# Kernel optimization log

Hardware: AMD Instinct MI355X
Metric: run time of the kernel (lower is better)

The kernel has to match this reference:

```python
import jax, jax.numpy as jnp
import numpy as np

ALPHA = 0.2  # LeakyReLU negative slope
NHEADS = 3
N = 100000
DEG = 32
NFEAT = 256
NHID = 64
NCLASS = 40


def _gat_layer(x, dst, src, W, a_dst, a_src, concat):
    # SpGraphAttentionLayer: h = x @ W; e_ij = exp(-leakyrelu(a1.h_i + a2.h_j));
    # out_i = sum_j e_ij h_j / sum_j e_ij  (edge (i,j) has dst=i, src=j)
    n = x.shape[0]
    h = x @ W                                   # [N, F']
    logits = (h @ a_dst)[dst] + (h @ a_src)[src]  # [E]
    e = jnp.exp(-jax.nn.leaky_relu(logits, ALPHA))  # [E]
    denom = jax.ops.segment_sum(e, dst, num_segments=n)            # [N]
    num = jax.ops.segment_sum(e[:, None] * h[src], dst, num_segments=n)  # [N, F']
    out = num / (denom[:, None] + 1e-16)
    return jax.nn.elu(out) if concat else out


def setup_inputs() -> dict:
    key = jax.random.key(0)
    ks = jax.random.split(key, 8)
    x = jax.random.normal(ks[0], (N, NFEAT), dtype=jnp.float32)
    # random edges + self-loops so every node has at least one incoming edge
    rnd = jax.random.randint(ks[1], (2, N * DEG), 0, N, dtype=jnp.int64)
    loops = jnp.tile(jnp.arange(N, dtype=jnp.int64)[None, :], (2, 1))
    edge_index = jnp.concatenate([rnd, loops], axis=1)  # [2, E]
    s = 1.0 / np.sqrt(NFEAT)
    W = jax.random.uniform(ks[2], (NHEADS, NFEAT, NHID), jnp.float32, -s, s)
    a1 = jax.random.uniform(ks[3], (NHEADS, NHID), jnp.float32, -s, s)
    a2 = jax.random.uniform(ks[4], (NHEADS, NHID), jnp.float32, -s, s)
    s2 = 1.0 / np.sqrt(NHEADS * NHID)
    W_out = jax.random.uniform(ks[5], (NHEADS * NHID, NCLASS), jnp.float32, -s2, s2)
    a1_out = jax.random.uniform(ks[6], (NCLASS,), jnp.float32, -s2, s2)
    a2_out = jax.random.uniform(ks[7], (NCLASS,), jnp.float32, -s2, s2)
    return {"x": x, "edge_index": edge_index, "W": W, "a1": a1, "a2": a2,
            "W_out": W_out, "a1_out": a1_out, "a2_out": a2_out}


def reference(x, edge_index, W, a1, a2, W_out, a1_out, a2_out):
    # eval mode: dropout is identity
    dst, src = edge_index[0], edge_index[1]
    heads = [_gat_layer(x, dst, src, W[k], a1[k], a2[k], concat=True)
             for k in range(NHEADS)]
    h = jnp.concatenate(heads, axis=1)  # [N, NHEADS*NHID]
    out = _gat_layer(h, dst, src, W_out, a1_out, a2_out, concat=False)
    return jax.nn.elu(out)  # [N, NCLASS]
```

## Files before the change

kernel.cpp:

```cpp
#include <hip/hip_runtime.h>

#define ALPHA 0.2f
#define NFEAT 256
#define NHID 64
#define NHEADS 3
#define NCLASS 40

#define CSRB 256
#define LDSW 12512
#define NP8  (LDSW * 8)

typedef short short8 __attribute__((ext_vector_type(8)));
typedef float float4v __attribute__((ext_vector_type(4)));
typedef _Float16 half4_t __attribute__((ext_vector_type(4)));

__device__ __forceinline__ float lrelu_negexp(float x) {
    float l = fmaxf(x, 0.f) + ALPHA * fminf(x, 0.f);
    return __expf(-l);
}
__device__ __forceinline__ float elu1(float x) {
    return x > 0.f ? x : (__expf(x) - 1.f);
}
__device__ __forceinline__ unsigned short f2bf(float f) {
    unsigned int u = __float_as_uint(f);
    unsigned int r = (u + 0x7FFFu + ((u >> 16) & 1u)) >> 16;
    return (unsigned short)r;
}
__device__ __forceinline__ float bf2f(unsigned short h) {
    return __uint_as_float(((unsigned int)h) << 16);
}
__device__ __forceinline__ float rdlane_f(float v, int l) {
    return __uint_as_float((unsigned)__builtin_amdgcn_readlane((int)__float_as_uint(v), l));
}

__global__ __launch_bounds__(256) void cvt_w_k(const float* __restrict__ W,
        unsigned short* __restrict__ wthi, unsigned short* __restrict__ wtlo) {
    int i = blockIdx.x * 256 + threadIdx.x;
    if (i >= NHEADS * NHID * NFEAT) return;
    int k = i & 255, nc = (i >> 8) & 63, head = i >> 14;
    float v = W[(size_t)head * NFEAT * NHID + (size_t)k * NHID + nc];
    unsigned short hi = f2bf(v);
    unsigned short lo = f2bf(v - bf2f(hi));
    wthi[i] = hi;
    wtlo[i] = lo;
}

__global__ __launch_bounds__(256) void gemm1_mfma_k(
        const float* __restrict__ x,
        const unsigned short* __restrict__ wthi, const unsigned short* __restrict__ wtlo,
        _Float16* __restrict__ h1h, int N) {
    __shared__ unsigned short Ah[128 * 40];
    __shared__ unsigned short Al[128 * 40];
    __shared__ unsigned short Bh[192 * 40];
    __shared__ unsigned short Bl[192 * 40];
    const int tid = threadIdx.x;
    const int wave = tid >> 6, lane = tid & 63;
    const int quad = lane >> 4, l16 = lane & 15;
    const int row0 = blockIdx.x * 128;
    const int wm = (wave >> 1) * 64;
    const int wn = (wave & 1) * 96;

    float4v acc[4][6];
#pragma unroll
    for (int s = 0; s < 4; ++s)
#pragma unroll
        for (int t = 0; t < 6; ++t)
            acc[s][t] = (float4v){0.f, 0.f, 0.f, 0.f};

    for (int kc = 0; kc < NFEAT; kc += 32) {
#pragma unroll
        for (int rr = 0; rr < 2; ++rr) {
            int idx = rr * 256 + tid;
            int r = idx >> 2, kq = (idx & 3) * 8;
            int gr = row0 + r; if (gr >= N) gr = N - 1;
            const float* xp = x + (size_t)gr * NFEAT + kc + kq;
            float4 f0 = *(const float4*)xp;
            float4 f1 = *(const float4*)(xp + 4);
            ushort4 h0, h1v, l0, l1;
            h0.x = f2bf(f0.x); l0.x = f2bf(f0.x - bf2f(h0.x));
            h0.y = f2bf(f0.y); l0.y = f2bf(f0.y - bf2f(h0.y));
            h0.z = f2bf(f0.z); l0.z = f2bf(f0.z - bf2f(h0.z));
            h0.w = f2bf(f0.w); l0.w = f2bf(f0.w - bf2f(h0.w));
            h1v.x = f2bf(f1.x); l1.x = f2bf(f1.x - bf2f(h1v.x));
            h1v.y = f2bf(f1.y); l1.y = f2bf(f1.y - bf2f(h1v.y));
            h1v.z = f2bf(f1.z); l1.z = f2bf(f1.z - bf2f(h1v.z));
            h1v.w = f2bf(f1.w); l1.w = f2bf(f1.w - bf2f(h1v.w));
            *(ushort4*)&Ah[r * 40 + kq]     = h0;
            *(ushort4*)&Ah[r * 40 + kq + 4] = h1v;
            *(ushort4*)&Al[r * 40 + kq]     = l0;
            *(ushort4*)&Al[r * 40 + kq + 4] = l1;
        }
#pragma unroll
        for (int rr = 0; rr < 3; ++rr) {
            int idx = rr * 256 + tid;
            int r = idx >> 2, kq = (idx & 3) * 8;
            size_t g = (size_t)r * NFEAT + kc + kq;
            *(int4*)&Bh[r * 40 + kq] = *(const int4*)(wthi + g);
            *(int4*)&Bl[r * 40 + kq] = *(const int4*)(wtlo + g);
        }
        __syncthreads();

        short8 ah[4], al[4];
#pragma unroll
        for (int s = 0; s < 4; ++s) {
            int m = wm + s * 16 + l16;
            ah[s] = *(const short8*)&Ah[m * 40 + quad * 8];
            al[s] = *(const short8*)&Al[m * 40 + quad * 8];
        }
#pragma unroll
        for (int t = 0; t < 6; ++t) {
            int n = wn + t * 16 + l16;
            short8 bh = *(const short8*)&Bh[n * 40 + quad * 8];
            short8 bl = *(const short8*)&Bl[n * 40 + quad * 8];
#pragma unroll
            for (int s = 0; s < 4; ++s) {
                acc[s][t] = __builtin_amdgcn_mfma_f32_16x16x32_bf16(ah[s], bh, acc[s][t], 0, 0, 0);
                acc[s][t] = __builtin_amdgcn_mfma_f32_16x16x32_bf16(ah[s], bl, acc[s][t], 0, 0, 0);
                acc[s][t] = __builtin_amdgcn_mfma_f32_16x16x32_bf16(al[s], bh, acc[s][t], 0, 0, 0);
            }
        }
        __syncthreads();
    }
#pragma unroll
    for (int s = 0; s < 4; ++s) {
#pragma unroll
        for (int r = 0; r < 4; ++r) {
            int grow = row0 + wm + s * 16 + quad * 4 + r;
            if (grow < N) {
#pragma unroll
                for (int t = 0; t < 6; ++t)
                    h1h[(size_t)grow * 192 + wn + t * 16 + l16] = (_Float16)acc[s][t][r];
            }
        }
    }
}

__global__ __launch_bounds__(256) void dots1_k(const _Float16* __restrict__ h1h,
        const float* __restrict__ a1, const float* __restrict__ a2,
        float* __restrict__ ad4, float* __restrict__ as4, int N) {
    int gt = blockIdx.x * 256 + threadIdx.x;
    int wid = gt >> 6, lane = gt & 63;
    if (wid >= N) return;
    const _Float16* hr = h1h + (size_t)wid * 192;
#pragma unroll
    for (int k = 0; k < 3; ++k) {
        float v = (float)hr[k*64 + lane];
        float da = v * a1[k*64 + lane];
        float db = v * a2[k*64 + lane];
#pragma unroll
        for (int o = 32; o > 0; o >>= 1) {
            da += __shfl_down(da, o, 64);
            db += __shfl_down(db, o, 64);
        }
        if (lane == 0) { ad4[wid*4+k] = da; as4[wid*4+k] = db; }
    }
}

__global__ __launch_bounds__(256) void hist_nib_k(const int* __restrict__ dst,
        unsigned* __restrict__ partial, int E) {
    __shared__ unsigned nib[LDSW];
    const int b = blockIdx.x, tid = threadIdx.x;
    for (int i = tid; i < LDSW; i += 256) nib[i] = 0u;
    __syncthreads();
    int chunk = (E + CSRB - 1) / CSRB;
    int e0 = b * chunk, e1 = min(E, e0 + chunk);
    for (int e = e0 + tid; e < e1; e += 256) {
        int d = dst[e];
        atomicAdd(&nib[d >> 3], 1u << ((d & 7) * 4));
    }
    __syncthreads();
    unsigned* p = partial + (size_t)b * LDSW;
    for (int i = tid; i < LDSW; i += 256) p[i] = nib[i];
}

__global__ __launch_bounds__(256) void bscan_k(const unsigned* __restrict__ partial,
        unsigned char* __restrict__ prefix8, int* __restrict__ cnt, int N) {
    int w = blockIdx.x * 256 + threadIdx.x;
    if (w >= LDSW) return;
    unsigned run[8];
#pragma unroll
    for (int n = 0; n < 8; ++n) run[n] = 0u;
    for (int b = 0; b < CSRB; ++b) {
        unsigned v = partial[(size_t)b * LDSW + w];
        unsigned lo = run[0] | (run[1] << 8) | (run[2] << 16) | (run[3] << 24);
        unsigned hi = run[4] | (run[5] << 8) | (run[6] << 16) | (run[7] << 24);
        *(uint2*)(prefix8 + (size_t)b * NP8 + (size_t)w * 8) = make_uint2(lo, hi);
#pragma unroll
        for (int n = 0; n < 8; ++n) run[n] += (v >> (n * 4)) & 15u;
    }
#pragma unroll
    for (int n = 0; n < 8; ++n) {
        int idx = w * 8 + n;
        if (idx < N) cnt[idx] = (int)run[n];
    }
}

__global__ __launch_bounds__(256) void scan1_k(const int* __restrict__ cnt,
        int* __restrict__ part, int* __restrict__ sums, int N) {
    __shared__ int s[256];
    int tid = threadIdx.x, b = blockIdx.x;
    int base = b * 2048 + tid * 8;
    int v[8]; int t = 0;
#pragma unroll
    for (int i = 0; i < 8; ++i) { int idx = base + i; v[i] = (idx < N) ? cnt[idx] : 0; t += v[i]; }
    s[tid] = t; __syncthreads();
    for (int o = 1; o < 256; o <<= 1) {
        int u = (tid >= o) ? s[tid - o] : 0;
        __syncthreads();
        s[tid] += u;
        __syncthreads();
    }
    int run = s[tid] - t;
#pragma unroll
    for (int i = 0; i < 8; ++i) { int idx = base + i; if (idx < N) part[idx] = run; run += v[i]; }
    if (tid == 255) sums[b] = s[255];
}

__global__ void scan2_k(int* sums, int nb) {
    if (threadIdx.x == 0 && blockIdx.x == 0) {
        int run = 0;
        for (int i = 0; i < nb; ++i) { int t = sums[i]; sums[i] = run; run += t; }
    }
}

__global__ __launch_bounds__(256) void scan3_k(const int* __restrict__ part,
        const int* __restrict__ sums, int* __restrict__ ptr, int N, int E) {
    int i = blockIdx.x * 256 + threadIdx.x;
    if (i < N) ptr[i] = part[i] + sums[i >> 11];
    if (i == 0) ptr[N] = E;
}

__global__ __launch_bounds__(256) void scatter_nib_k(const int* __restrict__ dst,
        const int* __restrict__ src, const int* __restrict__ ptr,
        const unsigned char* __restrict__ prefix8, int* __restrict__ csr, int E) {
    __shared__ unsigned nib[LDSW];
    const int b = blockIdx.x, tid = threadIdx.x;
    for (int i = tid; i < LDSW; i += 256) nib[i] = 0u;
    __syncthreads();
    const unsigned char* pb = prefix8 + (size_t)b * NP8;
    int chunk = (E + CSRB - 1) / CSRB;
    int e0 = b * chunk, e1 = min(E, e0 + chunk);
    for (int e = e0 + tid; e < e1; e += 256) {
        int d = dst[e];
        unsigned old = atomicAdd(&nib[d >> 3], 1u << ((d & 7) * 4));
        int local = (int)((old >> ((d & 7) * 4)) & 15u);
        csr[ptr[d] + (int)pb[d] + local] = src[e];
    }
}

__global__ __launch_bounds__(256) void agg1f_k(const _Float16* __restrict__ h1h,
        const float4* __restrict__ ad4, const float4* __restrict__ as4,
        const int* __restrict__ ptr, const int* __restrict__ csr,
        _Float16* __restrict__ out1h, int N) {
    int gt = blockIdx.x * 256 + threadIdx.x;
    int wid = gt >> 6, lane = gt & 63;
    if (wid >= N) return;
    int p0 = __builtin_amdgcn_readfirstlane(ptr[wid]);
    int p1 = __builtin_amdgcn_readfirstlane(ptr[wid + 1]);
    float4 ad = ad4[wid];
    const _Float16* hb = h1h + lane;
    float acc0 = 0.f, acc1 = 0.f, acc2 = 0.f;
    float dx = 0.f, dy = 0.f, dz = 0.f;

    for (int b0 = p0; b0 < p1; b0 += 64) {
        int e = b0 + lane;
        int cnt = min(64, p1 - b0);
        int si = 0; float wx = 0.f, wy = 0.f, wz = 0.f;
        if (e < p1) {
            si = csr[e];
            float4 as = as4[si];
            wx = lrelu_negexp(ad.x + as.x);
            wy = lrelu_negexp(ad.y + as.y);
            wz = lrelu_negexp(ad.z + as.z);
            dx += wx; dy += wy; dz += wz;
        }
        int jn = cnt & ~7;
        for (int j = 0; j < jn; j += 8) {
            float va[8], vb[8], vc[8], wxr[8], wyr[8], wzr[8];
#pragma unroll
            for (int i = 0; i < 8; ++i) {
                int s = __builtin_amdgcn_readlane(si, j + i);
                wxr[i] = rdlane_f(wx, j + i);
                wyr[i] = rdlane_f(wy, j + i);
                wzr[i] = rdlane_f(wz, j + i);
                const _Float16* hp = hb + (size_t)s * 192;
                va[i] = (float)hp[0];
                vb[i] = (float)hp[64];
                vc[i] = (float)hp[128];
            }
#pragma unroll
            for (int i = 0; i < 8; ++i) {
                acc0 = fmaf(wxr[i], va[i], acc0);
                acc1 = fmaf(wyr[i], vb[i], acc1);
                acc2 = fmaf(wzr[i], vc[i], acc2);
            }
        }
        for (int j = jn; j < cnt; ++j) {
            int s = __builtin_amdgcn_readlane(si, j);
            float wxx = rdlane_f(wx, j), wyy = rdlane_f(wy, j), wzz = rdlane_f(wz, j);
            const _Float16* hp = hb + (size_t)s * 192;
            acc0 = fmaf(wxx, (float)hp[0], acc0);
            acc1 = fmaf(wyy, (float)hp[64], acc1);
            acc2 = fmaf(wzz, (float)hp[128], acc2);
        }
    }

#pragma unroll
    for (int o = 32; o > 0; o >>= 1) {
        dx += __shfl_xor(dx, o, 64);
        dy += __shfl_xor(dy, o, 64);
        dz += __shfl_xor(dz, o, 64);
    }
    size_t ob = (size_t)wid * 192;
    out1h[ob + lane]       = (_Float16)elu1(acc0 / (dx + 1e-16f));
    out1h[ob + 64 + lane]  = (_Float16)elu1(acc1 / (dy + 1e-16f));
    out1h[ob + 128 + lane] = (_Float16)elu1(acc2 / (dz + 1e-16f));
}

__global__ __launch_bounds__(256) void gemm2_k(const _Float16* __restrict__ X,
        const float* __restrict__ Wo, _Float16* __restrict__ h2h, int N) {
    __shared__ float Xs[32][193];
    __shared__ float Ws[192 * 40];
    const int tid = threadIdx.x;
    const int row0 = blockIdx.x * 32;
    for (int i = tid; i < 192 * 40; i += 256) Ws[i] = Wo[i];
    for (int i = tid; i < 32 * 48; i += 256) {
        int r = i / 48, c4 = (i % 48) * 4;
        int rr = row0 + r; if (rr >= N) rr = N - 1;
        half4_t v = *(const half4_t*)(X + (size_t)rr * 192 + c4);
        Xs[r][c4+0] = (float)v.x; Xs[r][c4+1] = (float)v.y;
        Xs[r][c4+2] = (float)v.z; Xs[r][c4+3] = (float)v.w;
    }
    __syncthreads();
    int rsub = tid >> 3;
    int f0 = (tid & 7) * 5;
    float acc[5] = {0, 0, 0, 0, 0};
    for (int c = 0; c < 192; ++c) {
        float xv = Xs[rsub][c];
#pragma unroll
        for (int j = 0; j < 5; ++j) acc[j] = fmaf(xv, Ws[c*40 + f0 + j], acc[j]);
    }
    int r = row0 + rsub;
    if (r < N) {
#pragma unroll
        for (int j = 0; j < 5; ++j) h2h[(size_t)r*64 + f0 + j] = (_Float16)acc[j];
    }
}

__global__ __launch_bounds__(256) void dots2_k(const _Float16* __restrict__ h2h,
        const float* __restrict__ a1o, const float* __restrict__ a2o,
        float* __restrict__ ad2, float* __restrict__ as2, int N) {
    int gt = blockIdx.x * 256 + threadIdx.x;
    int wid = gt >> 6, lane = gt & 63;
    if (wid >= N) return;
    float v = 0.f, w1 = 0.f, w2 = 0.f;
    if (lane < 40) { v = (float)h2h[(size_t)wid*64 + lane]; w1 = a1o[lane]; w2 = a2o[lane]; }
    float da = v * w1, db = v * w2;
#pragma unroll
    for (int o = 32; o > 0; o >>= 1) { da += __shfl_down(da, o, 64); db += __shfl_down(db, o, 64); }
    if (lane == 0) { ad2[wid] = da; as2[wid] = db; }
}

__global__ __launch_bounds__(256) void agg2f_k(const _Float16* __restrict__ h2h,
        const float* __restrict__ ad2, const float* __restrict__ as2,
        const int* __restrict__ ptr, const int* __restrict__ csr,
        float* __restrict__ out, int N) {
    int gt = blockIdx.x * 256 + threadIdx.x;
    int wid = gt >> 6, lane = gt & 63;
    if (wid >= N) return;
    int p0 = __builtin_amdgcn_readfirstlane(ptr[wid]);
    int p1 = __builtin_amdgcn_readfirstlane(ptr[wid + 1]);
    float ad = ad2[wid];
    const _Float16* hb = h2h + lane;
    float acc = 0.f, den = 0.f;

    for (int b0 = p0; b0 < p1; b0 += 64) {
        int e = b0 + lane;
        int cnt = min(64, p1 - b0);
        int si = 0; float w = 0.f;
        if (e < p1) {
            si = csr[e];
            w = lrelu_negexp(ad + as2[si]);
            den += w;
        }
        int jn = cnt & ~7;
        for (int j = 0; j < jn; j += 8) {
            float v[8], cw[8];
#pragma unroll
            for (int i = 0; i < 8; ++i) {
                int s = __builtin_amdgcn_readlane(si, j + i);
                cw[i] = rdlane_f(w, j + i);
                v[i] = (float)hb[(size_t)s * 64];
            }
#pragma unroll
            for (int i = 0; i < 8; ++i) acc = fmaf(cw[i], v[i], acc);
        }
        for (int j = jn; j < cnt; ++j) {
            int s = __builtin_amdgcn_readlane(si, j);
            float cw = rdlane_f(w, j);
            acc = fmaf(cw, (float)hb[(size_t)s * 64], acc);
        }
    }

#pragma unroll
    for (int o = 32; o > 0; o >>= 1) den += __shfl_xor(den, o, 64);
    if (lane < 40) {
        out[(size_t)wid * 40 + lane] = elu1(acc / (den + 1e-16f));
    }
}

extern "C" void kernel_launch(void* const* d_in, const int* in_sizes, int n_in,
                              void* d_out, int out_size, void* d_ws, size_t ws_size,
                              hipStream_t stream) {
    const float* x   = (const float*)d_in[0];
    const int*   ei  = (const int*)d_in[1];
    const float* W   = (const float*)d_in[2];
    const float* a1  = (const float*)d_in[3];
    const float* a2  = (const float*)d_in[4];
    const float* Wo  = (const float*)d_in[5];
    const float* a1o = (const float*)d_in[6];
    const float* a2o = (const float*)d_in[7];
    const int N = in_sizes[0] / NFEAT;
    const int E = in_sizes[1] / 2;
    const int* dst = ei;
    const int* src = ei + E;

    char* base = (char*)d_ws;
    size_t off = 0;
    auto alloc = [&](size_t bytes) { void* p = base + off; off += (bytes + 255) & ~(size_t)255; return p; };
    _Float16* h1h   = (_Float16*)alloc((size_t)N * 192 * 2);
    _Float16* out1h = (_Float16*)alloc((size_t)N * 192 * 2);
    int*      csr   = (int*)alloc((size_t)E * 4);
    unsigned* partial = (unsigned*)alloc((size_t)CSRB * LDSW * 4);
    unsigned char* prefix8 = (unsigned char*)alloc((size_t)CSRB * NP8);
    char*     bufA  = (char*)alloc((size_t)N * 144 + 4096);
    int*      ptr   = (int*)alloc((size_t)(N + 1) * 4);
    int*      cnt   = (int*)alloc((size_t)N * 4);
    int*      part  = (int*)alloc((size_t)N * 4);
    int*      sums  = (int*)alloc(1024);
    float*    ad4   = (float*)alloc((size_t)N * 4 * 4);
    float*    as4   = (float*)alloc((size_t)N * 4 * 4);
    unsigned short* wthi = (unsigned short*)alloc((size_t)NHEADS * NHID * NFEAT * 2);
    unsigned short* wtlo = (unsigned short*)alloc((size_t)NHEADS * NHID * NFEAT * 2);

    _Float16* h2h = (_Float16*)bufA;
    float*    ad2 = (float*)(bufA + (size_t)N * 128 + 1024);
    float*    as2 = ad2 + N;

    cvt_w_k<<<(NHEADS * NHID * NFEAT + 255) / 256, 256, 0, stream>>>(W, wthi, wtlo);
    gemm1_mfma_k<<<(N + 127) / 128, 256, 0, stream>>>(x, wthi, wtlo, h1h, N);

    hist_nib_k<<<CSRB, 256, 0, stream>>>(dst, partial, E);
    bscan_k<<<(LDSW + 255) / 256, 256, 0, stream>>>(partial, prefix8, cnt, N);
    int nb = (N + 2047) / 2048;
    scan1_k<<<nb, 256, 0, stream>>>(cnt, part, sums, N);
    scan2_k<<<1, 64, 0, stream>>>(sums, nb);
    scan3_k<<<(N + 255) / 256, 256, 0, stream>>>(part, sums, ptr, N, E);
    scatter_nib_k<<<CSRB, 256, 0, stream>>>(dst, src, ptr, prefix8, csr, E);

    dots1_k<<<(N + 3) / 4, 256, 0, stream>>>(h1h, a1, a2, ad4, as4, N);
    agg1f_k<<<(N + 3) / 4, 256, 0, stream>>>(h1h, (const float4*)ad4,
                                             (const float4*)as4, ptr, csr, out1h, N);

    gemm2_k<<<(N + 31) / 32, 256, 0, stream>>>(out1h, Wo, h2h, N);
    dots2_k<<<(N + 3) / 4, 256, 0, stream>>>(h2h, a1o, a2o, ad2, as2, N);
    agg2f_k<<<(N + 3) / 4, 256, 0, stream>>>(h2h, ad2, as2, ptr, csr, (float*)d_out, N);
}
```

Before: 817.3 us.

## Parallelize block prefix scan, fuse layer-2 attention dots into gemm2, unroll agg2

Splits the serial 256-block column scan into a two-level scan: 16 groups of 16 blocks scanned in parallel, then a group-level scan, with the scatter adding both offsets. This gives the scan far more threads than the 12512 it had before. It also folds the dots2 kernel into gemm2's epilogue with an 8-lane shuffle reduction, which removes one launch and a full reread of h2h. agg2's gather loop is unrolled from 8 to 16 to expose more loads in flight, at the cost of more registers and extra scratch buffers.

```diff
diff --git a/kernel.cpp b/kernel.cpp
--- a/kernel.cpp
+++ b/kernel.cpp
@@ -9,6 +9,7 @@
 #define CSRB 256
 #define LDSW 12512
 #define NP8  (LDSW * 8)
+#define NGRP 16
 
 typedef short short8 __attribute__((ext_vector_type(8)));
 typedef float float4v __attribute__((ext_vector_type(4)));
@@ -173,20 +174,46 @@
     for (int i = tid; i < LDSW; i += 256) p[i] = nib[i];
 }
 
-__global__ __launch_bounds__(256) void bscan_k(const unsigned* __restrict__ partial,
-        unsigned char* __restrict__ prefix8, int* __restrict__ cnt, int N) {
-    int w = blockIdx.x * 256 + threadIdx.x;
-    if (w >= LDSW) return;
+__global__ __launch_bounds__(256) void bscan1_k(const unsigned* __restrict__ partial,
+        unsigned char* __restrict__ prefix8, unsigned char* __restrict__ gsum8) {
+    int t = blockIdx.x * 256 + threadIdx.x;
+    if (t >= LDSW * NGRP) return;
+    int g = t / LDSW, w = t - g * LDSW;
     unsigned run[8];
 #pragma unroll
     for (int n = 0; n < 8; ++n) run[n] = 0u;
-    for (int b = 0; b < CSRB; ++b) {
+#pragma unroll
+    for (int j = 0; j < 16; ++j) {
+        int b = g * 16 + j;
         unsigned v = partial[(size_t)b * LDSW + w];
         unsigned lo = run[0] | (run[1] << 8) | (run[2] << 16) | (run[3] << 24);
         unsigned hi = run[4] | (run[5] << 8) | (run[6] << 16) | (run[7] << 24);
         *(uint2*)(prefix8 + (size_t)b * NP8 + (size_t)w * 8) = make_uint2(lo, hi);
 #pragma unroll
         for (int n = 0; n < 8; ++n) run[n] += (v >> (n * 4)) & 15u;
+    }
+    unsigned lo = run[0] | (run[1] << 8) | (run[2] << 16) | (run[3] << 24);
+    unsigned hi = run[4] | (run[5] << 8) | (run[6] << 16) | (run[7] << 24);
+    *(uint2*)(gsum8 + (size_t)g * NP8 + (size_t)w * 8) = make_uint2(lo, hi);
+}
+
+__global__ __launch_bounds__(256) void bscan2_k(const unsigned char* __restrict__ gsum8,
+        unsigned char* __restrict__ gpre8, int* __restrict__ cnt, int N) {
+    int w = blockIdx.x * 256 + threadIdx.x;
+    if (w >= LDSW) return;
+    unsigned run[8];
+#pragma unroll
+    for (int n = 0; n < 8; ++n) run[n] = 0u;
+#pragma unroll
+    for (int g = 0; g < NGRP; ++g) {
+        uint2 v = *(const uint2*)(gsum8 + (size_t)g * NP8 + (size_t)w * 8);
+        unsigned lo = run[0] | (run[1] << 8) | (run[2] << 16) | (run[3] << 24);
+        unsigned hi = run[4] | (run[5] << 8) | (run[6] << 16) | (run[7] << 24);
+        *(uint2*)(gpre8 + (size_t)g * NP8 + (size_t)w * 8) = make_uint2(lo, hi);
+        run[0] += v.x & 255u;         run[1] += (v.x >> 8) & 255u;
+        run[2] += (v.x >> 16) & 255u; run[3] += (v.x >> 24) & 255u;
+        run[4] += v.y & 255u;         run[5] += (v.y >> 8) & 255u;
+        run[6] += (v.y >> 16) & 255u; run[7] += (v.y >> 24) & 255u;
     }
 #pragma unroll
     for (int n = 0; n < 8; ++n) {
@@ -232,19 +259,21 @@
 
 __global__ __launch_bounds__(256) void scatter_nib_k(const int* __restrict__ dst,
         const int* __restrict__ src, const int* __restrict__ ptr,
-        const unsigned char* __restrict__ prefix8, int* __restrict__ csr, int E) {
+        const unsigned char* __restrict__ prefix8, const unsigned char* __restrict__ gpre8,
+        int* __restrict__ csr, int E) {
     __shared__ unsigned nib[LDSW];
     const int b = blockIdx.x, tid = threadIdx.x;
     for (int i = tid; i < LDSW; i += 256) nib[i] = 0u;
     __syncthreads();
     const unsigned char* pb = prefix8 + (size_t)b * NP8;
+    const unsigned char* gp = gpre8 + (size_t)(b >> 4) * NP8;
     int chunk = (E + CSRB - 1) / CSRB;
     int e0 = b * chunk, e1 = min(E, e0 + chunk);
     for (int e = e0 + tid; e < e1; e += 256) {
         int d = dst[e];
         unsigned old = atomicAdd(&nib[d >> 3], 1u << ((d & 7) * 4));
         int local = (int)((old >> ((d & 7) * 4)) & 15u);
-        csr[ptr[d] + (int)pb[d] + local] = src[e];
+        csr[ptr[d] + (int)gp[d] + (int)pb[d] + local] = src[e];
     }
 }
 
@@ -318,7 +347,9 @@
 }
 
 __global__ __launch_bounds__(256) void gemm2_k(const _Float16* __restrict__ X,
-        const float* __restrict__ Wo, _Float16* __restrict__ h2h, int N) {
+        const float* __restrict__ Wo, const float* __restrict__ a1o,
+        const float* __restrict__ a2o, _Float16* __restrict__ h2h,
+        float* __restrict__ ad2, float* __restrict__ as2, int N) {
     __shared__ float Xs[32][193];
     __shared__ float Ws[192 * 40];
     const int tid = threadIdx.x;
@@ -342,23 +373,21 @@
     }
     int r = row0 + rsub;
     if (r < N) {
-#pragma unroll
-        for (int j = 0; j < 5; ++j) h2h[(size_t)r*64 + f0 + j] = (_Float16)acc[j];
-    }
-}
-
-__global__ __launch_bounds__(256) void dots2_k(const _Float16* __restrict__ h2h,
-        const float* __restrict__ a1o, const float* __restrict__ a2o,
-        float* __restrict__ ad2, float* __restrict__ as2, int N) {
-    int gt = blockIdx.x * 256 + threadIdx.x;
-    int wid = gt >> 6, lane = gt & 63;
-    if (wid >= N) return;
-    float v = 0.f, w1 = 0.f, w2 = 0.f;
-    if (lane < 40) { v = (float)h2h[(size_t)wid*64 + lane]; w1 = a1o[lane]; w2 = a2o[lane]; }
-    float da = v * w1, db = v * w2;
-#pragma unroll
-    for (int o = 32; o > 0; o >>= 1) { da += __shfl_down(da, o, 64); db += __shfl_down(db, o, 64); }
-    if (lane == 0) { ad2[wid] = da; as2[wid] = db; }
+        float da = 0.f, db = 0.f;
+#pragma unroll
+        for (int j = 0; j < 5; ++j) {
+            h2h[(size_t)r*64 + f0 + j] = (_Float16)acc[j];
+            float hv = (float)(_Float16)acc[j];
+            da = fmaf(hv, a1o[f0 + j], da);
+            db = fmaf(hv, a2o[f0 + j], db);
+        }
+#pragma unroll
+        for (int o = 4; o > 0; o >>= 1) {
+            da += __shfl_down(da, o, 8);
+            db += __shfl_down(db, o, 8);
+        }
+        if ((tid & 7) == 0) { ad2[r] = da; as2[r] = db; }
+    }
 }
 
 __global__ __launch_bounds__(256) void agg2f_k(const _Float16* __restrict__ h2h,
@@ -383,17 +412,17 @@
             w = lrelu_negexp(ad + as2[si]);
             den += w;
         }
-        int jn = cnt & ~7;
-        for (int j = 0; j < jn; j += 8) {
-            float v[8], cw[8];
-#pragma unroll
-            for (int i = 0; i < 8; ++i) {
+        int jn = cnt & ~15;
+        for (int j = 0; j < jn; j += 16) {
+            float v[16], cw[16];
+#pragma unroll
+            for (int i = 0; i < 16; ++i) {
                 int s = __builtin_amdgcn_readlane(si, j + i);
                 cw[i] = rdlane_f(w, j + i);
                 v[i] = (float)hb[(size_t)s * 64];
             }
 #pragma unroll
-            for (int i = 0; i < 8; ++i) acc = fmaf(cw[i], v[i], acc);
+            for (int i = 0; i < 16; ++i) acc = fmaf(cw[i], v[i], acc);
         }
         for (int j = jn; j < cnt; ++j) {
             int s = __builtin_amdgcn_readlane(si, j);
@@ -433,6 +462,8 @@
     int*      csr   = (int*)alloc((size_t)E * 4);
     unsigned* partial = (unsigned*)alloc((size_t)CSRB * LDSW * 4);
     unsigned char* prefix8 = (unsigned char*)alloc((size_t)CSRB * NP8);
+    unsigned char* gsum8   = (unsigned char*)alloc((size_t)NGRP * NP8);
+    unsigned char* gpre8   = (unsigned char*)alloc((size_t)NGRP * NP8);
     char*     bufA  = (char*)alloc((size_t)N * 144 + 4096);
     int*      ptr   = (int*)alloc((size_t)(N + 1) * 4);
     int*      cnt   = (int*)alloc((size_t)N * 4);
@@ -451,18 +482,18 @@
     gemm1_mfma_k<<<(N + 127) / 128, 256, 0, stream>>>(x, wthi, wtlo, h1h, N);
 
     hist_nib_k<<<CSRB, 256, 0, stream>>>(dst, partial, E);
-    bscan_k<<<(LDSW + 255) / 256, 256, 0, stream>>>(partial, prefix8, cnt, N);
+    bscan1_k<<<(LDSW * NGRP + 255) / 256, 256, 0, stream>>>(partial, prefix8, gsum8);
+    bscan2_k<<<(LDSW + 255) / 256, 256, 0, stream>>>(gsum8, gpre8, cnt, N);
     int nb = (N + 2047) / 2048;
     scan1_k<<<nb, 256, 0, stream>>>(cnt, part, sums, N);
     scan2_k<<<1, 64, 0, stream>>>(sums, nb);
     scan3_k<<<(N + 255) / 256, 256, 0, stream>>>(part, sums, ptr, N, E);
-    scatter_nib_k<<<CSRB, 256, 0, stream>>>(dst, src, ptr, prefix8, csr, E);
+    scatter_nib_k<<<CSRB, 256, 0, stream>>>(dst, src, ptr, prefix8, gpre8, csr, E);
 
     dots1_k<<<(N + 3) / 4, 256, 0, stream>>>(h1h, a1, a2, ad4, as4, N);
     agg1f_k<<<(N + 3) / 4, 256, 0, stream>>>(h1h, (const float4*)ad4,
                                              (const float4*)as4, ptr, csr, out1h, N);
 
-    gemm2_k<<<(N + 31) / 32, 256, 0, stream>>>(out1h, Wo, h2h, N);
-    dots2_k<<<(N + 3) / 4, 256, 0, stream>>>(h2h, a1o, a2o, ad2, as2, N);
+    gemm2_k<<<(N + 31) / 32, 256, 0, stream>>>(out1h, Wo, a1o, a2o, h2h, ad2, as2, N);
     agg2f_k<<<(N + 3) / 4, 256, 0, stream>>>(h2h, ad2, as2, ptr, csr, (float*)d_out, N);
 }
```

New measurement: 791.9 us. 3.1% less time.
